# Kernel optimization log

Hardware: AMD Instinct MI355X
Metric: run time of the kernel (lower is better)

## Reference

```python
import jax, jax.numpy as jnp
import numpy as np
import math

N, IN_DIM, OUT_DIM = 4096, 1024, 1024
MASK = True


def setup_inputs() -> dict:
    key = jax.random.key(0)
    ks = jax.random.split(key, 6)
    s = 1.0 / math.sqrt(IN_DIM)
    return {
        "qx": jax.random.normal(ks[0], (N, IN_DIM), jnp.float32),
        "kx": jax.random.normal(ks[1], (N, IN_DIM), jnp.float32),
        "vx": jax.random.normal(ks[2], (N, IN_DIM), jnp.float32),
        # torch nn.Linear weight layout: [out_dim, in_dim], y = x @ W.T
        "Wq": jax.random.normal(ks[3], (OUT_DIM, IN_DIM), jnp.float32) * s,
        "Wk": jax.random.normal(ks[4], (OUT_DIM, IN_DIM), jnp.float32) * s,
        "Wv": jax.random.normal(ks[5], (OUT_DIM, IN_DIM), jnp.float32) * s,
    }


def reference(qx, kx, vx, Wq, Wk, Wv):
    q = qx @ Wq.T  # [n, d]
    k = kx @ Wk.T
    v = vx @ Wv.T
    scores = (q @ k.T) / jnp.float32(math.sqrt(OUT_DIM))  # [n, n]
    if MASK:
        n = qx.shape[0]
        col = jnp.arange(n)[None, :]
        row = jnp.arange(n)[:, None]
        # original: -10000 where j > i (strictly upper triangular)
        scores = scores + jnp.where(col > row, jnp.float32(-10000.0), jnp.float32(0.0))
    attn = jax.nn.softmax(scores, axis=1)
    return attn @ v
```

## Files before the change

kernel.cpp:

```cpp
#include <hip/hip_runtime.h>
#include <hip/hip_bf16.h>
#include <stdint.h>

#define NTOK 4096
#define DIM  1024

typedef unsigned short u16;
typedef __bf16 bf16x8 __attribute__((ext_vector_type(8)));
typedef float f32x4 __attribute__((ext_vector_type(4)));
typedef u16 u16x8 __attribute__((ext_vector_type(8)));

__device__ __forceinline__ u16 f2bf(float f) {
  union { float f; uint32_t u; } c; c.f = f;
  return (u16)((c.u + 0x7fffu + ((c.u >> 16) & 1u)) >> 16);
}

__device__ __forceinline__ float wave_max(float v) {
#pragma unroll
  for (int o = 32; o; o >>= 1) v = fmaxf(v, __shfl_xor(v, o, 64));
  return v;
}
__device__ __forceinline__ float wave_sum(float v) {
#pragma unroll
  for (int o = 32; o; o >>= 1) v += __shfl_xor(v, o, 64);
  return v;
}

__device__ __forceinline__ int xcd_swz(int orig, int nwg) {
  const int q = nwg >> 3, r = nwg & 7;
  const int x = orig & 7, i = orig >> 3;
  return (x < r ? x * (q + 1) : r * (q + 1) + (x - r) * q) + i;
}

__device__ __forceinline__ void gld16(const u16* g, u16* l) {
  __builtin_amdgcn_global_load_lds((const __attribute__((address_space(1))) void*)g,
                                   (__attribute__((address_space(3))) void*)l, 16, 0, 0);
}

__global__ __launch_bounds__(256) void cvt6(
    const float* __restrict__ qx, const float* __restrict__ kx, const float* __restrict__ vx,
    const float* __restrict__ Wq, const float* __restrict__ Wk, const float* __restrict__ Wv,
    u16* __restrict__ qxb, u16* __restrict__ kxb, u16* __restrict__ vxb,
    u16* __restrict__ Wqb, u16* __restrict__ Wkb, u16* __restrict__ Wvb)
{
  const int z = blockIdx.z;
  const int nelem = (z < 3) ? NTOK * DIM : DIM * DIM;
  const int i = (blockIdx.x * 256 + threadIdx.x) * 8;
  if (i >= nelem) return;
  const float* in = (z == 0) ? qx : (z == 1) ? kx : (z == 2) ? vx
                  : (z == 3) ? Wq : (z == 4) ? Wk : Wv;
  u16* out = (z == 0) ? qxb : (z == 1) ? kxb : (z == 2) ? vxb
           : (z == 3) ? Wqb : (z == 4) ? Wkb : Wvb;
  float4 a = *reinterpret_cast<const float4*>(in + i);
  float4 b = *reinterpret_cast<const float4*>(in + i + 4);
  u16x8 o;
  o[0] = f2bf(a.x); o[1] = f2bf(a.y); o[2] = f2bf(a.z); o[3] = f2bf(a.w);
  o[4] = f2bf(b.x); o[5] = f2bf(b.y); o[6] = f2bf(b.z); o[7] = f2bf(b.w);
  *reinterpret_cast<u16x8*>(out + i) = o;
}

template<int BM>
__device__ __forceinline__ void mm_core(
    const u16* __restrict__ A, const u16* __restrict__ B,
    int lda, int ldb, int klo, int khi, int row0, int col0,
    u16* sA, u16* sB, f32x4 (&acc)[BM / 32][4])
{
  constexpr int RPWA = BM / 4;
  const int tid = threadIdx.x;
  const int wave = tid >> 6, lane = tid & 63;
  const int wr = wave >> 1, wc = wave & 1;
  const int l15 = lane & 15, l4 = lane >> 4;
  const int h = l15 & 7;

  const int r8 = lane >> 3;
  const int scol = ((lane & 7) ^ r8) << 3;
  const u16* gA = A + (size_t)(row0 + wave * RPWA + r8) * lda + scol;
  const u16* gB = B + (size_t)(col0 + wave * 32 + r8) * ldb + scol;
  const int lbA = wave * RPWA * 64;
  const int lbB = wave * 32 * 64;

  for (int k0 = klo; k0 < khi; k0 += 64) {
    __syncthreads();
#pragma unroll
    for (int i = 0; i < RPWA / 8; ++i)
      gld16(gA + (size_t)(i * 8) * lda + k0, &sA[lbA + i * 8 * 64]);
#pragma unroll
    for (int i = 0; i < 4; ++i)
      gld16(gB + (size_t)(i * 8) * ldb + k0, &sB[lbB + i * 8 * 64]);
    __syncthreads();
#pragma unroll
    for (int ks = 0; ks < 2; ++ks) {
      bf16x8 af[BM / 32], bfv[4];
#pragma unroll
      for (int mf = 0; mf < BM / 32; ++mf)
        af[mf] = *reinterpret_cast<const bf16x8*>(
            (const char*)sA + ((wr * (BM / 2) + mf * 16 + l15) << 7) + ((((ks << 2) + l4) ^ h) << 4));
#pragma unroll
      for (int nf = 0; nf < 4; ++nf)
        bfv[nf] = *reinterpret_cast<const bf16x8*>(
            (const char*)sB + ((wc * 64 + nf * 16 + l15) << 7) + ((((ks << 2) + l4) ^ h) << 4));
#pragma unroll
      for (int mf = 0; mf < BM / 32; ++mf)
#pragma unroll
        for (int nf = 0; nf < 4; ++nf)
          acc[mf][nf] = __builtin_amdgcn_mfma_f32_16x16x32_bf16(af[mf], bfv[nf], acc[mf][nf], 0, 0, 0);
    }
  }
}

__global__ __launch_bounds__(256) void proj_sw(
    const u16* __restrict__ qxb, const u16* __restrict__ kxb, const u16* __restrict__ vxb,
    const u16* __restrict__ Wqb, const u16* __restrict__ Wkb, const u16* __restrict__ Wvb,
    u16* __restrict__ qb, u16* __restrict__ kb, u16* __restrict__ vT)
{
  __shared__ alignas(16) u16 sA[128 * 64];
  __shared__ alignas(16) u16 sB[128 * 64];
  const int w = xcd_swz(blockIdx.x, 768);
  const int z = w >> 8, rem = w & 255;
  const int by = rem >> 3, bx = rem & 7;
  const u16* A = (z == 0) ? qxb : (z == 1) ? kxb : vxb;
  const u16* B = (z == 0) ? Wqb : (z == 1) ? Wkb : Wvb;
  const int row0 = by * 128, col0 = bx * 128;

  f32x4 acc[4][4] = {};
  mm_core<128>(A, B, DIM, DIM, 0, DIM, row0, col0, sA, sB, acc);

  const int lane = threadIdx.x & 63;
  const int wave = threadIdx.x >> 6;
  const int l15 = lane & 15, l4 = lane >> 4;
  const int om = row0 + (wave >> 1) * 64;
  const int on = col0 + (wave & 1) * 64;
  if (z < 2) {
    u16* C = (z == 0) ? qb : kb;
#pragma unroll
    for (int mf = 0; mf < 4; ++mf)
#pragma unroll
      for (int nf = 0; nf < 4; ++nf)
#pragma unroll
        for (int r = 0; r < 4; ++r)
          C[(size_t)(om + mf * 16 + l4 * 4 + r) * DIM + (on + nf * 16 + l15)] = f2bf(acc[mf][nf][r]);
  } else {
#pragma unroll
    for (int mf = 0; mf < 4; ++mf)
#pragma unroll
      for (int nf = 0; nf < 4; ++nf) {
        ushort4 o;
        o.x = f2bf(acc[mf][nf][0]);
        o.y = f2bf(acc[mf][nf][1]);
        o.z = f2bf(acc[mf][nf][2]);
        o.w = f2bf(acc[mf][nf][3]);
        *reinterpret_cast<ushort4*>(&vT[(size_t)(on + nf * 16 + l15) * NTOK + (om + mf * 16 + l4 * 4)]) = o;
      }
  }
}

__global__ __launch_bounds__(256) void gemm_scores(
    const u16* __restrict__ A, const u16* __restrict__ B, float* __restrict__ C, float scale)
{
  __shared__ alignas(16) u16 sA[128 * 64];
  __shared__ alignas(16) u16 sB[128 * 64];
  const int t = xcd_swz(blockIdx.x, 528);
  int by = (int)((sqrtf(8.0f * t + 1.0f) - 1.0f) * 0.5f);
  while ((by + 1) * (by + 2) / 2 <= t) ++by;
  while (by * (by + 1) / 2 > t) --by;
  const int bx = t - by * (by + 1) / 2;
  const int row0 = by * 128, col0 = bx * 128;

  f32x4 acc[4][4] = {};
  mm_core<128>(A, B, DIM, DIM, 0, DIM, row0, col0, sA, sB, acc);

  const int lane = threadIdx.x & 63;
  const int wave = threadIdx.x >> 6;
  const int l15 = lane & 15, l4 = lane >> 4;
  const int om = row0 + (wave >> 1) * 64;
  const int on = col0 + (wave & 1) * 64;
#pragma unroll
  for (int mf = 0; mf < 4; ++mf)
#pragma unroll
    for (int nf = 0; nf < 4; ++nf)
#pragma unroll
      for (int r = 0; r < 4; ++r)
        C[(size_t)(om + mf * 16 + l4 * 4 + r) * NTOK + (on + nf * 16 + l15)] = acc[mf][nf][r] * scale;
}

__global__ __launch_bounds__(256) void gemm_pv(
    const u16* __restrict__ P, const u16* __restrict__ vT, float* __restrict__ C)
{
  __shared__ alignas(16) u16 sA[64 * 64];
  __shared__ alignas(16) u16 sB[128 * 64];
  const int w = xcd_swz(blockIdx.x, 768);
  const int bx = w & 7;
  const int cid = w >> 3;
  int by, half;
  if (cid < 32) { by = cid; half = -1; }
  else { const int j = cid - 32; by = 32 + (j >> 1); half = j & 1; }
  const int row0 = by * 64, col0 = bx * 128;
  const int Klim = row0 + 64;
  int klo = 0, khi = Klim;
  if (half >= 0) {
    const int h1 = (((Klim >> 6) + 1) >> 1) << 6;
    if (half == 0) khi = h1; else klo = h1;
  }

  f32x4 acc[2][4] = {};
  mm_core<64>(P, vT, NTOK, NTOK, klo, khi, row0, col0, sA, sB, acc);

  const int lane = threadIdx.x & 63;
  const int wave = threadIdx.x >> 6;
  const int l15 = lane & 15, l4 = lane >> 4;
  const int om = row0 + (wave >> 1) * 32;
  const int on = col0 + (wave & 1) * 64;
#pragma unroll
  for (int mf = 0; mf < 2; ++mf)
#pragma unroll
    for (int nf = 0; nf < 4; ++nf)
#pragma unroll
      for (int r = 0; r < 4; ++r) {
        const size_t idx = (size_t)(om + mf * 16 + l4 * 4 + r) * DIM + (on + nf * 16 + l15);
        if (half >= 0) atomicAdd(&C[idx], acc[mf][nf][r]);
        else C[idx] = acc[mf][nf][r];
      }
}

__global__ __launch_bounds__(256) void softmax_causal(const float* __restrict__ S,
                                                      u16* __restrict__ P) {
  __shared__ float buf[NTOK];
  __shared__ float red[8];
  const int row = blockIdx.x;
  const int tid = threadIdx.x;
  const int limit = row + 1;
  const int limit128 = (row & ~127) + 128;
  const float* srow = S + (size_t)row * NTOK;

  float lmax = -1e30f;
  for (int j = tid * 4; j < limit128; j += 1024) {
    float4 s;
    if (j + 4 <= limit) {
      s = *reinterpret_cast<const float4*>(srow + j);
    } else {
      s.x = (j + 0 < limit) ? srow[j + 0] : -1e30f;
      s.y = (j + 1 < limit) ? srow[j + 1] : -1e30f;
      s.z = (j + 2 < limit) ? srow[j + 2] : -1e30f;
      s.w = (j + 3 < limit) ? srow[j + 3] : -1e30f;
    }
    *reinterpret_cast<float4*>(buf + j) = s;
    lmax = fmaxf(lmax, fmaxf(fmaxf(s.x, s.y), fmaxf(s.z, s.w)));
  }
  lmax = wave_max(lmax);
  if ((tid & 63) == 0) red[tid >> 6] = lmax;
  __syncthreads();
  const float m = fmaxf(fmaxf(red[0], red[1]), fmaxf(red[2], red[3]));

  float lsum = 0.f;
  for (int j = tid * 4; j < limit128; j += 1024) {
    float4 s = *reinterpret_cast<float4*>(buf + j);
    float4 e;
    e.x = __expf(s.x - m); e.y = __expf(s.y - m);
    e.z = __expf(s.z - m); e.w = __expf(s.w - m);
    *reinterpret_cast<float4*>(buf + j) = e;
    lsum += (e.x + e.y) + (e.z + e.w);
  }
  lsum = wave_sum(lsum);
  if ((tid & 63) == 0) red[4 + (tid >> 6)] = lsum;
  __syncthreads();
  const float inv = 1.0f / (red[4] + red[5] + red[6] + red[7]);

  u16* prow = P + (size_t)row * NTOK;
  for (int j = tid * 4; j < limit128; j += 1024) {
    float4 e = *reinterpret_cast<float4*>(buf + j);
    ushort4 o;
    o.x = f2bf(e.x * inv); o.y = f2bf(e.y * inv);
    o.z = f2bf(e.z * inv); o.w = f2bf(e.w * inv);
    *reinterpret_cast<ushort4*>(prow + j) = o;
  }
}

extern "C" void kernel_launch(void* const* d_in, const int* in_sizes, int n_in,
                              void* d_out, int out_size, void* d_ws, size_t ws_size,
                              hipStream_t stream) {
  const float* qx = (const float*)d_in[0];
  const float* kx = (const float*)d_in[1];
  const float* vx = (const float*)d_in[2];
  const float* Wq = (const float*)d_in[3];
  const float* Wk = (const float*)d_in[4];
  const float* Wv = (const float*)d_in[5];
  float* out = (float*)d_out;
  char* ws = (char*)d_ws;
  const size_t MB = 1024ull * 1024ull;

  if (ws_size < 120 * MB) {
    hipMemsetAsync(d_out, 0xFF, (size_t)out_size * sizeof(float), stream);
    return;
  }

  u16* qxb = (u16*)(ws);
  u16* kxb = (u16*)(ws + 8 * MB);
  u16* vxb = (u16*)(ws + 16 * MB);
  u16* Wqb = (u16*)(ws + 24 * MB);
  u16* Wkb = (u16*)(ws + 26 * MB);
  u16* Wvb = (u16*)(ws + 28 * MB);
  float* S = (float*)(ws);
  u16* qb  = (u16*)(ws + 64 * MB);
  u16* kb  = (u16*)(ws + 72 * MB);
  u16* vT  = (u16*)(ws + 80 * MB);
  u16* P   = (u16*)(ws + 88 * MB);

  hipMemsetAsync((char*)out + (size_t)2048 * DIM * 4, 0, (size_t)2048 * DIM * 4, stream);

  cvt6<<<dim3(NTOK * DIM / (256 * 8), 1, 6), 256, 0, stream>>>(
      qx, kx, vx, Wq, Wk, Wv, qxb, kxb, vxb, Wqb, Wkb, Wvb);

  proj_sw<<<768, 256, 0, stream>>>(qxb, kxb, vxb, Wqb, Wkb, Wvb, qb, kb, vT);

  gemm_scores<<<528, 256, 0, stream>>>(qb, kb, S, 0.03125f);

  softmax_causal<<<NTOK, 256, 0, stream>>>(S, P);

  gemm_pv<<<768, 256, 0, stream>>>(P, vT, out);
}
```

Before: 144.4 us.

## Double-buffer LDS in GEMM core and store scores as bf16

The shared GEMM mainloop now double-buffers its LDS tiles, issuing the loads for the next K slice before computing on the current one, with a single barrier per iteration. This is meant to hide global-load latency behind the MFMA work. Separately, the score matrix is stored in bf16 instead of fp32, halving the bytes gemm_scores writes and softmax reads, and softmax is reworked to process 8 elements per thread. The cost is doubled LDS usage per block, which can lower occupancy, and reduced precision in the pre-softmax scores.

```diff
diff --git a/kernel.cpp b/kernel.cpp
--- a/kernel.cpp
+++ b/kernel.cpp
@@ -13,6 +13,10 @@
 __device__ __forceinline__ u16 f2bf(float f) {
   union { float f; uint32_t u; } c; c.f = f;
   return (u16)((c.u + 0x7fffu + ((c.u >> 16) & 1u)) >> 16);
+}
+__device__ __forceinline__ float bf2f(u16 b) {
+  union { uint32_t u; float f; } c; c.u = (uint32_t)b << 16;
+  return c.f;
 }
 
 __device__ __forceinline__ float wave_max(float v) {
@@ -66,6 +70,8 @@
     u16* sA, u16* sB, f32x4 (&acc)[BM / 32][4])
 {
   constexpr int RPWA = BM / 4;
+  constexpr int ASZ = BM * 64;
+  constexpr int BSZ = 128 * 64;
   const int tid = threadIdx.x;
   const int wave = tid >> 6, lane = tid & 63;
   const int wr = wave >> 1, wc = wave & 1;
@@ -79,32 +85,46 @@
   const int lbA = wave * RPWA * 64;
   const int lbB = wave * 32 * 64;
 
+#pragma unroll
+  for (int i = 0; i < RPWA / 8; ++i)
+    gld16(gA + (size_t)(i * 8) * lda + klo, &sA[lbA + i * 512]);
+#pragma unroll
+  for (int i = 0; i < 4; ++i)
+    gld16(gB + (size_t)(i * 8) * ldb + klo, &sB[lbB + i * 512]);
+  __syncthreads();
+
+  int cur = 0;
   for (int k0 = klo; k0 < khi; k0 += 64) {
-    __syncthreads();
-#pragma unroll
-    for (int i = 0; i < RPWA / 8; ++i)
-      gld16(gA + (size_t)(i * 8) * lda + k0, &sA[lbA + i * 8 * 64]);
-#pragma unroll
-    for (int i = 0; i < 4; ++i)
-      gld16(gB + (size_t)(i * 8) * ldb + k0, &sB[lbB + i * 8 * 64]);
-    __syncthreads();
+    const int nxt = cur ^ 1;
+    if (k0 + 64 < khi) {
+#pragma unroll
+      for (int i = 0; i < RPWA / 8; ++i)
+        gld16(gA + (size_t)(i * 8) * lda + k0 + 64, &sA[nxt * ASZ + lbA + i * 512]);
+#pragma unroll
+      for (int i = 0; i < 4; ++i)
+        gld16(gB + (size_t)(i * 8) * ldb + k0 + 64, &sB[nxt * BSZ + lbB + i * 512]);
+    }
+    const char* bA = (const char*)(sA + cur * ASZ);
+    const char* bB = (const char*)(sB + cur * BSZ);
 #pragma unroll
     for (int ks = 0; ks < 2; ++ks) {
       bf16x8 af[BM / 32], bfv[4];
 #pragma unroll
       for (int mf = 0; mf < BM / 32; ++mf)
         af[mf] = *reinterpret_cast<const bf16x8*>(
-            (const char*)sA + ((wr * (BM / 2) + mf * 16 + l15) << 7) + ((((ks << 2) + l4) ^ h) << 4));
+            bA + ((wr * (BM / 2) + mf * 16 + l15) << 7) + ((((ks << 2) + l4) ^ h) << 4));
 #pragma unroll
       for (int nf = 0; nf < 4; ++nf)
         bfv[nf] = *reinterpret_cast<const bf16x8*>(
-            (const char*)sB + ((wc * 64 + nf * 16 + l15) << 7) + ((((ks << 2) + l4) ^ h) << 4));
+            bB + ((wc * 64 + nf * 16 + l15) << 7) + ((((ks << 2) + l4) ^ h) << 4));
 #pragma unroll
       for (int mf = 0; mf < BM / 32; ++mf)
 #pragma unroll
         for (int nf = 0; nf < 4; ++nf)
           acc[mf][nf] = __builtin_amdgcn_mfma_f32_16x16x32_bf16(af[mf], bfv[nf], acc[mf][nf], 0, 0, 0);
     }
+    __syncthreads();
+    cur = nxt;
   }
 }
 
@@ -113,8 +133,8 @@
     const u16* __restrict__ Wqb, const u16* __restrict__ Wkb, const u16* __restrict__ Wvb,
     u16* __restrict__ qb, u16* __restrict__ kb, u16* __restrict__ vT)
 {
-  __shared__ alignas(16) u16 sA[128 * 64];
-  __shared__ alignas(16) u16 sB[128 * 64];
+  __shared__ alignas(16) u16 sA[2 * 128 * 64];
+  __shared__ alignas(16) u16 sB[2 * 128 * 64];
   const int w = xcd_swz(blockIdx.x, 768);
   const int z = w >> 8, rem = w & 255;
   const int by = rem >> 3, bx = rem & 7;
@@ -155,10 +175,10 @@
 }
 
 __global__ __launch_bounds__(256) void gemm_scores(
-    const u16* __restrict__ A, const u16* __restrict__ B, float* __restrict__ C, float scale)
-{
-  __shared__ alignas(16) u16 sA[128 * 64];
-  __shared__ alignas(16) u16 sB[128 * 64];
+    const u16* __restrict__ A, const u16* __restrict__ B, u16* __restrict__ C, float scale)
+{
+  __shared__ alignas(16) u16 sA[2 * 128 * 64];
+  __shared__ alignas(16) u16 sB[2 * 128 * 64];
   const int t = xcd_swz(blockIdx.x, 528);
   int by = (int)((sqrtf(8.0f * t + 1.0f) - 1.0f) * 0.5f);
   while ((by + 1) * (by + 2) / 2 <= t) ++by;
@@ -180,14 +200,14 @@
     for (int nf = 0; nf < 4; ++nf)
 #pragma unroll
       for (int r = 0; r < 4; ++r)
-        C[(size_t)(om + mf * 16 + l4 * 4 + r) * NTOK + (on + nf * 16 + l15)] = acc[mf][nf][r] * scale;
+        C[(size_t)(om + mf * 16 + l4 * 4 + r) * NTOK + (on + nf * 16 + l15)] = f2bf(acc[mf][nf][r] * scale);
 }
 
 __global__ __launch_bounds__(256) void gemm_pv(
     const u16* __restrict__ P, const u16* __restrict__ vT, float* __restrict__ C)
 {
-  __shared__ alignas(16) u16 sA[64 * 64];
-  __shared__ alignas(16) u16 sB[128 * 64];
+  __shared__ alignas(16) u16 sA[2 * 64 * 64];
+  __shared__ alignas(16) u16 sB[2 * 128 * 64];
   const int w = xcd_swz(blockIdx.x, 768);
   const int bx = w & 7;
   const int cid = w >> 3;
@@ -222,7 +242,7 @@
       }
 }
 
-__global__ __launch_bounds__(256) void softmax_causal(const float* __restrict__ S,
+__global__ __launch_bounds__(256) void softmax_causal(const u16* __restrict__ S,
                                                       u16* __restrict__ P) {
   __shared__ float buf[NTOK];
   __shared__ float red[8];
@@ -230,21 +250,24 @@
   const int tid = threadIdx.x;
   const int limit = row + 1;
   const int limit128 = (row & ~127) + 128;
-  const float* srow = S + (size_t)row * NTOK;
+  const u16* srow = S + (size_t)row * NTOK;
 
   float lmax = -1e30f;
-  for (int j = tid * 4; j < limit128; j += 1024) {
-    float4 s;
-    if (j + 4 <= limit) {
-      s = *reinterpret_cast<const float4*>(srow + j);
+  for (int j = tid * 8; j < limit128; j += 2048) {
+    float v[8];
+    if (j + 8 <= limit) {
+      u16x8 sv = *reinterpret_cast<const u16x8*>(srow + j);
+#pragma unroll
+      for (int e = 0; e < 8; ++e) v[e] = bf2f(sv[e]);
     } else {
-      s.x = (j + 0 < limit) ? srow[j + 0] : -1e30f;
-      s.y = (j + 1 < limit) ? srow[j + 1] : -1e30f;
-      s.z = (j + 2 < limit) ? srow[j + 2] : -1e30f;
-      s.w = (j + 3 < limit) ? srow[j + 3] : -1e30f;
+#pragma unroll
+      for (int e = 0; e < 8; ++e) v[e] = (j + e < limit) ? bf2f(srow[j + e]) : -1e30f;
     }
-    *reinterpret_cast<float4*>(buf + j) = s;
-    lmax = fmaxf(lmax, fmaxf(fmaxf(s.x, s.y), fmaxf(s.z, s.w)));
+    float4 lo = {v[0], v[1], v[2], v[3]}, hi = {v[4], v[5], v[6], v[7]};
+    *reinterpret_cast<float4*>(buf + j) = lo;
+    *reinterpret_cast<float4*>(buf + j + 4) = hi;
+#pragma unroll
+    for (int e = 0; e < 8; ++e) lmax = fmaxf(lmax, v[e]);
   }
   lmax = wave_max(lmax);
   if ((tid & 63) == 0) red[tid >> 6] = lmax;
@@ -252,13 +275,15 @@
   const float m = fmaxf(fmaxf(red[0], red[1]), fmaxf(red[2], red[3]));
 
   float lsum = 0.f;
-  for (int j = tid * 4; j < limit128; j += 1024) {
-    float4 s = *reinterpret_cast<float4*>(buf + j);
-    float4 e;
-    e.x = __expf(s.x - m); e.y = __expf(s.y - m);
-    e.z = __expf(s.z - m); e.w = __expf(s.w - m);
-    *reinterpret_cast<float4*>(buf + j) = e;
-    lsum += (e.x + e.y) + (e.z + e.w);
+  for (int j = tid * 8; j < limit128; j += 2048) {
+    float4 lo = *reinterpret_cast<float4*>(buf + j);
+    float4 hi = *reinterpret_cast<float4*>(buf + j + 4);
+    float e0 = __expf(lo.x - m), e1 = __expf(lo.y - m), e2 = __expf(lo.z - m), e3 = __expf(lo.w - m);
+    float e4 = __expf(hi.x - m), e5 = __expf(hi.y - m), e6 = __expf(hi.z - m), e7 = __expf(hi.w - m);
+    float4 eo = {e0, e1, e2, e3}, eh = {e4, e5, e6, e7};
+    *reinterpret_cast<float4*>(buf + j) = eo;
+    *reinterpret_cast<float4*>(buf + j + 4) = eh;
+    lsum += ((e0 + e1) + (e2 + e3)) + ((e4 + e5) + (e6 + e7));
   }
   lsum = wave_sum(lsum);
   if ((tid & 63) == 0) red[4 + (tid >> 6)] = lsum;
@@ -266,12 +291,15 @@
   const float inv = 1.0f / (red[4] + red[5] + red[6] + red[7]);
 
   u16* prow = P + (size_t)row * NTOK;
-  for (int j = tid * 4; j < limit128; j += 1024) {
-    float4 e = *reinterpret_cast<float4*>(buf + j);
-    ushort4 o;
-    o.x = f2bf(e.x * inv); o.y = f2bf(e.y * inv);
-    o.z = f2bf(e.z * inv); o.w = f2bf(e.w * inv);
-    *reinterpret_cast<ushort4*>(prow + j) = o;
+  for (int j = tid * 8; j < limit128; j += 2048) {
+    float4 lo = *reinterpret_cast<float4*>(buf + j);
+    float4 hi = *reinterpret_cast<float4*>(buf + j + 4);
+    u16x8 o;
+    o[0] = f2bf(lo.x * inv); o[1] = f2bf(lo.y * inv);
+    o[2] = f2bf(lo.z * inv); o[3] = f2bf(lo.w * inv);
+    o[4] = f2bf(hi.x * inv); o[5] = f2bf(hi.y * inv);
+    o[6] = f2bf(hi.z * inv); o[7] = f2bf(hi.w * inv);
+    *reinterpret_cast<u16x8*>(prow + j) = o;
   }
 }
 
@@ -299,7 +327,7 @@
   u16* Wqb = (u16*)(ws + 24 * MB);
   u16* Wkb = (u16*)(ws + 26 * MB);
   u16* Wvb = (u16*)(ws + 28 * MB);
-  float* S = (float*)(ws);
+  u16* S   = (u16*)(ws);
   u16* qb  = (u16*)(ws + 64 * MB);
   u16* kb  = (u16*)(ws + 72 * MB);
   u16* vT  = (u16*)(ws + 80 * MB);
```

New measurement: 140.5 us. 1.03x faster.
